# Optimization experiments

Measured on AMD Instinct MI355X. Metric: run time of the kernel, lower is better.

The kernel has to match this reference:

```python
import jax, jax.numpy as jnp
import numpy as np

B, H, W, CIN = 16, 64, 64, 64
KWH, COUT, NSAMPLE = 3, 128, 8


def setup_inputs() -> dict:
    key = jax.random.key(0)
    k1, k2, k3, k4 = jax.random.split(key, 4)
    x = jax.random.normal(k1, (B, H, W, CIN), dtype=jnp.float32)
    mu = jax.random.normal(k2, (KWH, KWH, CIN, COUT), dtype=jnp.float32)
    logstd = jax.random.normal(k3, (KWH, KWH, CIN, COUT), dtype=jnp.float32)
    noise = jax.random.normal(k4, (NSAMPLE, KWH, KWH, CIN, COUT), dtype=jnp.float32)
    return {"x": x, "mu": mu, "logstd": logstd, "noise": noise}


def reference(x, mu, logstd, noise):
    # Sampled kernels: [nsample, kh, kw, cin, cout]
    kernels = mu[None] + noise * jnp.exp(logstd)[None]

    def conv_one(k):
        y = jax.lax.conv_general_dilated(
            x, k, window_strides=(1, 1), padding='SAME',
            dimension_numbers=('NHWC', 'HWIO', 'NHWC'))
        return jax.nn.elu(y)

    # [nsample, B, H, W, cout] -> [B, H, W, nsample, cout]
    out = jax.vmap(conv_one)(kernels)
    return jnp.transpose(out, (1, 2, 3, 0, 4))
```

## Files before the change

### kernel.cpp

```cpp
#include <hip/hip_runtime.h>
#include <hip/hip_bf16.h>

typedef __attribute__((ext_vector_type(8))) short short8;
typedef __attribute__((ext_vector_type(4))) float floatx4;

#define AS_STRIDE 72

__global__ void sample_kernels_k(const float* __restrict__ mu,
                                 const float* __restrict__ logstd,
                                 const float* __restrict__ noise,
                                 __hip_bfloat16* __restrict__ kerF) {
  const int s = blockIdx.x / 9, tap = blockIdx.x % 9;
  const float* mu_p = mu + tap * 8192;
  const float* ls_p = logstd + tap * 8192;
  const float* nz_p = noise + (s * 9 + tap) * 8192;
  for (int f = threadIdx.x; f < 1024; f += 256) {
    int khalf = f >> 9;
    int nz = (f >> 6) & 7;
    int lane = f & 63;
    int co = nz * 16 + (lane & 15);
    int ci0 = khalf * 32 + ((lane >> 4) & 3) * 8;
    short8 frag;
#pragma unroll
    for (int j = 0; j < 8; ++j) {
      int idx = (ci0 + j) * 128 + co;
      float v = mu_p[idx] + nz_p[idx] * expf(ls_p[idx]);
      frag[j] = (short)__bfloat16_as_ushort(__float2bfloat16(v));
    }
    *(short8*)(kerF + ((size_t)((s * 18 + tap * 2 + khalf) * 8 + nz) * 64 + lane) * 8) = frag;
  }
}

__global__ __launch_bounds__(256, 4)
void conv_elu_k(const float* __restrict__ x,
                const __hip_bfloat16* __restrict__ kerF,
                float* __restrict__ out) {
  __shared__ __hip_bfloat16 As[4 * 66 * AS_STRIDE];

  const int tid = threadIdx.x;
  const int lane = tid & 63;
  const int lane15 = tid & 15;
  const int quad = (tid >> 4) & 3;
  const int wave = tid >> 6;
  const int n_tile = blockIdx.x;
  const int mt = blockIdx.y;
  const int b = mt >> 5;
  const int h0 = (mt & 31) << 1;

  const float* xb = x + (size_t)b * (64 * 64 * 64);
  for (int i = tid; i < 4 * 66 * 16; i += 256) {
    int r = i / (66 * 16);
    int rem = i - r * (66 * 16);
    int j = rem >> 4;
    int p = rem & 15;
    int h_in = h0 + r - 1;
    int w_in = j - 1;
    float4 v = make_float4(0.f, 0.f, 0.f, 0.f);
    if ((unsigned)h_in < 64u && (unsigned)w_in < 64u)
      v = *(const float4*)(xb + (((h_in << 6) + w_in) << 6) + (p << 2));
    ushort2 pk0 = {__bfloat16_as_ushort(__float2bfloat16(v.x)),
                   __bfloat16_as_ushort(__float2bfloat16(v.y))};
    ushort2 pk1 = {__bfloat16_as_ushort(__float2bfloat16(v.z)),
                   __bfloat16_as_ushort(__float2bfloat16(v.w))};
    *(ushort2*)&As[(r * 66 + j) * AS_STRIDE + (p << 2)] = pk0;
    *(ushort2*)&As[(r * 66 + j) * AS_STRIDE + (p << 2) + 2] = pk1;
  }

  floatx4 acc[4][4] = {};

  const int row_sel = wave >> 1;
  const int nz0 = (wave & 1) << 2;
  const __hip_bfloat16* bTile = kerF + (size_t)n_tile * 18 * 8 * 64 * 8;

  __syncthreads();

  short8 aC[4], bC[4], aN[4], bN[4];

  auto loadB = [&](short8* dst, int ks) {
#pragma unroll
    for (int ni = 0; ni < 4; ++ni)
      dst[ni] = *(const short8*)(bTile + ((size_t)(ks * 8 + nz0 + ni) * 64 + lane) * 8);
  };
  auto loadA = [&](short8* dst, int ks) {
    const int tap = ks >> 1, khalf = ks & 1;
    const int kh = tap / 3, kw = tap - kh * 3;
    const __hip_bfloat16* aBase =
        As + ((row_sel + kh) * 66 + kw + lane15) * AS_STRIDE + quad * 8 + khalf * 32;
#pragma unroll
    for (int mi = 0; mi < 4; ++mi)
      dst[mi] = *(const short8*)(aBase + mi * 16 * AS_STRIDE);
  };

  loadB(bC, 0);
  loadA(aC, 0);
#pragma unroll
  for (int ks = 0; ks < 18; ++ks) {
    if (ks < 17) {
      loadB(bN, ks + 1);
      loadA(aN, ks + 1);
    }
#pragma unroll
    for (int mi = 0; mi < 4; ++mi)
#pragma unroll
      for (int ni = 0; ni < 4; ++ni)
        acc[mi][ni] = __builtin_amdgcn_mfma_f32_16x16x32_bf16(
            aC[mi], bC[ni], acc[mi][ni], 0, 0, 0);
#pragma unroll
    for (int r = 0; r < 4; ++r) { aC[r] = aN[r]; bC[r] = bN[r]; }
  }

  const int h = h0 + row_sel;
  float* outp = out + (size_t)((b * 64 + h) * 64) * 1024 +
                (size_t)(n_tile * 128 + (nz0 << 4) + lane15);
#pragma unroll
  for (int mi = 0; mi < 4; ++mi) {
#pragma unroll
    for (int r = 0; r < 4; ++r) {
      int w = mi * 16 + quad * 4 + r;
      float* orow = outp + (size_t)w * 1024;
#pragma unroll
      for (int ni = 0; ni < 4; ++ni) {
        float v = acc[mi][ni][r];
        orow[ni * 16] = v > 0.f ? v : expm1f(v);
      }
    }
  }
}

extern "C" void kernel_launch(void* const* d_in, const int* in_sizes, int n_in,
                              void* d_out, int out_size, void* d_ws, size_t ws_size,
                              hipStream_t stream) {
  const float* x      = (const float*)d_in[0];
  const float* mu     = (const float*)d_in[1];
  const float* logstd = (const float*)d_in[2];
  const float* noise  = (const float*)d_in[3];
  float* out = (float*)d_out;
  __hip_bfloat16* kerF = (__hip_bfloat16*)d_ws;

  sample_kernels_k<<<72, 256, 0, stream>>>(mu, logstd, noise, kerF);
  conv_elu_k<<<dim3(8, 512), 256, 0, stream>>>(x, kerF, out);
}
```

Before: 381.3 us.

## Pre-convert input to padded bf16 buffer and deepen B-fragment prefetch

The prep kernel now also writes a zero-padded bf16 copy of x to workspace, so the conv kernel's tile load becomes plain 16-byte copies with no bounds checks or fp32-to-bf16 conversion. Previously each of the 8 n-tile blocks re-read and re-converted the same fp32 rows. The change adds one extra global write and read of the padded input, plus more workspace. The B-fragment prefetch also goes from one step ahead to two, which raises register pressure.

Result: faster. 342.8 us (-10.1%).

```diff
diff --git a/kernel.cpp b/kernel.cpp
--- a/kernel.cpp
+++ b/kernel.cpp
@@ -2,37 +2,68 @@
 #include <hip/hip_bf16.h>
 
 typedef __attribute__((ext_vector_type(8))) short short8;
+typedef __attribute__((ext_vector_type(8))) unsigned short ushort8;
 typedef __attribute__((ext_vector_type(4))) float floatx4;
 
 #define AS_STRIDE 72
 
-__global__ void sample_kernels_k(const float* __restrict__ mu,
-                                 const float* __restrict__ logstd,
-                                 const float* __restrict__ noise,
-                                 __hip_bfloat16* __restrict__ kerF) {
-  const int s = blockIdx.x / 9, tap = blockIdx.x % 9;
-  const float* mu_p = mu + tap * 8192;
-  const float* ls_p = logstd + tap * 8192;
-  const float* nz_p = noise + (s * 9 + tap) * 8192;
-  for (int f = threadIdx.x; f < 1024; f += 256) {
-    int khalf = f >> 9;
-    int nz = (f >> 6) & 7;
-    int lane = f & 63;
-    int co = nz * 16 + (lane & 15);
-    int ci0 = khalf * 32 + ((lane >> 4) & 3) * 8;
-    short8 frag;
+#define KERF_BYTES (1024 * 576 * 2)
+
+__global__ void prep_k(const float* __restrict__ x,
+                       const float* __restrict__ mu,
+                       const float* __restrict__ logstd,
+                       const float* __restrict__ noise,
+                       __hip_bfloat16* __restrict__ kerF,
+                       __hip_bfloat16* __restrict__ xpad) {
+  const int bx = blockIdx.x;
+  const int tid = threadIdx.x;
+  if (bx >= 72) {
+    int i = (bx - 72) * 256 + tid;
+    int row = i >> 3, seg = i & 7;
+    int b = row / 4356;
+    int rem = row - b * 4356;
+    int hp = rem / 66, wp = rem - (rem / 66) * 66;
+    int h = hp - 1, w = wp - 1;
+    ushort8 val = {0, 0, 0, 0, 0, 0, 0, 0};
+    if ((unsigned)h < 64u && (unsigned)w < 64u) {
+      const float* src = x + ((((size_t)b * 64 + h) * 64 + w) << 6) + (seg << 3);
+      float4 v0 = *(const float4*)src;
+      float4 v1 = *(const float4*)(src + 4);
+      val[0] = __bfloat16_as_ushort(__float2bfloat16(v0.x));
+      val[1] = __bfloat16_as_ushort(__float2bfloat16(v0.y));
+      val[2] = __bfloat16_as_ushort(__float2bfloat16(v0.z));
+      val[3] = __bfloat16_as_ushort(__float2bfloat16(v0.w));
+      val[4] = __bfloat16_as_ushort(__float2bfloat16(v1.x));
+      val[5] = __bfloat16_as_ushort(__float2bfloat16(v1.y));
+      val[6] = __bfloat16_as_ushort(__float2bfloat16(v1.z));
+      val[7] = __bfloat16_as_ushort(__float2bfloat16(v1.w));
+    }
+    *(ushort8*)(xpad + ((size_t)row << 6) + (seg << 3)) = val;
+  } else {
+    const int s = bx / 9, tap = bx % 9;
+    const float* mu_p = mu + tap * 8192;
+    const float* ls_p = logstd + tap * 8192;
+    const float* nz_p = noise + (s * 9 + tap) * 8192;
+    for (int f = tid; f < 1024; f += 256) {
+      int khalf = f >> 9;
+      int nz = (f >> 6) & 7;
+      int lane = f & 63;
+      int co = nz * 16 + (lane & 15);
+      int ci0 = khalf * 32 + ((lane >> 4) & 3) * 8;
+      short8 frag;
 #pragma unroll
-    for (int j = 0; j < 8; ++j) {
-      int idx = (ci0 + j) * 128 + co;
-      float v = mu_p[idx] + nz_p[idx] * expf(ls_p[idx]);
-      frag[j] = (short)__bfloat16_as_ushort(__float2bfloat16(v));
+      for (int j = 0; j < 8; ++j) {
+        int idx = (ci0 + j) * 128 + co;
+        float v = mu_p[idx] + nz_p[idx] * expf(ls_p[idx]);
+        frag[j] = (short)__bfloat16_as_ushort(__float2bfloat16(v));
+      }
+      *(short8*)(kerF + ((size_t)((s * 18 + tap * 2 + khalf) * 8 + nz) * 64 + lane) * 8) = frag;
     }
-    *(short8*)(kerF + ((size_t)((s * 18 + tap * 2 + khalf) * 8 + nz) * 64 + lane) * 8) = frag;
   }
 }
 
 __global__ __launch_bounds__(256, 4)
-void conv_elu_k(const float* __restrict__ x,
+void conv_elu_k(const __hip_bfloat16* __restrict__ xpad,
                 const __hip_bfloat16* __restrict__ kerF,
                 float* __restrict__ out) {
   __shared__ __hip_bfloat16 As[4 * 66 * AS_STRIDE];
@@ -47,23 +78,14 @@
   const int b = mt >> 5;
   const int h0 = (mt & 31) << 1;
 
-  const float* xb = x + (size_t)b * (64 * 64 * 64);
-  for (int i = tid; i < 4 * 66 * 16; i += 256) {
-    int r = i / (66 * 16);
-    int rem = i - r * (66 * 16);
-    int j = rem >> 4;
-    int p = rem & 15;
-    int h_in = h0 + r - 1;
-    int w_in = j - 1;
-    float4 v = make_float4(0.f, 0.f, 0.f, 0.f);
-    if ((unsigned)h_in < 64u && (unsigned)w_in < 64u)
-      v = *(const float4*)(xb + (((h_in << 6) + w_in) << 6) + (p << 2));
-    ushort2 pk0 = {__bfloat16_as_ushort(__float2bfloat16(v.x)),
-                   __bfloat16_as_ushort(__float2bfloat16(v.y))};
-    ushort2 pk1 = {__bfloat16_as_ushort(__float2bfloat16(v.z)),
-                   __bfloat16_as_ushort(__float2bfloat16(v.w))};
-    *(ushort2*)&As[(r * 66 + j) * AS_STRIDE + (p << 2)] = pk0;
-    *(ushort2*)&As[(r * 66 + j) * AS_STRIDE + (p << 2) + 2] = pk1;
+  const __hip_bfloat16* xbase = xpad + (((size_t)(b * 66 + h0) * 66) << 6);
+  for (int c = tid; c < 2112; c += 256) {
+    ushort8 v = *(const ushort8*)(xbase + ((size_t)c << 3));
+    int r = c / 528;
+    int cc = c - r * 528;
+    int j = cc >> 3;
+    int ci = (cc & 7) << 3;
+    *(ushort8*)&As[(r * 66 + j) * AS_STRIDE + ci] = v;
   }
 
   floatx4 acc[4][4] = {};
@@ -74,7 +96,7 @@
 
   __syncthreads();
 
-  short8 aC[4], bC[4], aN[4], bN[4];
+  short8 aCur[4], aNxt[4], b0[4], b1[4], b2[4];
 
   auto loadB = [&](short8* dst, int ks) {
 #pragma unroll
@@ -91,22 +113,25 @@
       dst[mi] = *(const short8*)(aBase + mi * 16 * AS_STRIDE);
   };
 
-  loadB(bC, 0);
-  loadA(aC, 0);
+  loadB(b0, 0);
+  loadB(b1, 1);
+  loadA(aCur, 0);
 #pragma unroll
   for (int ks = 0; ks < 18; ++ks) {
-    if (ks < 17) {
-      loadB(bN, ks + 1);
-      loadA(aN, ks + 1);
-    }
+    if (ks + 2 < 18) loadB(b2, ks + 2);
+    if (ks + 1 < 18) loadA(aNxt, ks + 1);
 #pragma unroll
     for (int mi = 0; mi < 4; ++mi)
 #pragma unroll
       for (int ni = 0; ni < 4; ++ni)
         acc[mi][ni] = __builtin_amdgcn_mfma_f32_16x16x32_bf16(
-            aC[mi], bC[ni], acc[mi][ni], 0, 0, 0);
+            aCur[mi], b0[ni], acc[mi][ni], 0, 0, 0);
 #pragma unroll
-    for (int r = 0; r < 4; ++r) { aC[r] = aN[r]; bC[r] = bN[r]; }
+    for (int r = 0; r < 4; ++r) {
+      aCur[r] = aNxt[r];
+      b0[r] = b1[r];
+      b1[r] = b2[r];
+    }
   }
 
   const int h = h0 + row_sel;
@@ -136,7 +161,8 @@
   const float* noise  = (const float*)d_in[3];
   float* out = (float*)d_out;
   __hip_bfloat16* kerF = (__hip_bfloat16*)d_ws;
+  __hip_bfloat16* xpad = (__hip_bfloat16*)((char*)d_ws + KERF_BYTES);
 
-  sample_kernels_k<<<72, 256, 0, stream>>>(mu, logstd, noise, kerF);
-  conv_elu_k<<<dim3(8, 512), 256, 0, stream>>>(x, kerF, out);
+  prep_k<<<2250, 256, 0, stream>>>(x, mu, logstd, noise, kerF, xpad);
+  conv_elu_k<<<dim3(8, 512), 256, 0, stream>>>(xpad, kerF, out);
 }
```
